# Kernel tuning notes

Measured on AMD Instinct MI355X. Metric: run time of the kernel, lower is better.

The kernel has to match this reference:

```python
import jax, jax.numpy as jnp
import numpy as np

T = 2048        # Tmax encoder frames
EPROJS = 1024   # encoder projection dim (Henc)
DUNITS = 512    # prediction net hidden
EMBED = 512     # embedding dim
JOINT = 512     # joint space dim
ODIM = 10000    # output vocab
BLANK = 0


def setup_inputs() -> dict:
    key = jax.random.key(0)
    ks = jax.random.split(key, 11)
    def g(k, shape, scale):
        return (jax.random.normal(k, shape, dtype=jnp.float32) * scale)
    inp = {
        'h': jax.random.normal(ks[0], (T, EPROJS), dtype=jnp.float32),
        # Embedding with padding_idx=blank -> blank row zeroed
        'embed': g(ks[1], (ODIM, EMBED), 0.05).at[BLANK].set(0.0),
        # LSTMCell params (torch gate order: i, f, g, o)
        'W_ih': g(ks[2], (4 * DUNITS, EMBED), 1.0 / np.sqrt(EMBED)),
        'W_hh': g(ks[3], (4 * DUNITS, DUNITS), 1.0 / np.sqrt(DUNITS)),
        'b_ih': g(ks[4], (4 * DUNITS,), 0.01),
        'b_hh': g(ks[5], (4 * DUNITS,), 0.01),
        # joint network
        'W_enc': g(ks[6], (JOINT, EPROJS), 1.0 / np.sqrt(EPROJS)),
        'b_enc': g(ks[7], (JOINT,), 0.01),
        'W_dec': g(ks[8], (JOINT, DUNITS), 1.0 / np.sqrt(DUNITS)),  # no bias
        'W_out': g(ks[9], (ODIM, JOINT), 1.0 / np.sqrt(JOINT)),
        'b_out': g(ks[10], (ODIM,), 0.01),
    }
    return inp


def _lstm_cell(x, h_prev, c_prev, W_ih, W_hh, b_ih, b_hh):
    gates = W_ih @ x + b_ih + W_hh @ h_prev + b_hh  # (4*DUNITS,)
    i, f, g, o = jnp.split(gates, 4)
    c = jax.nn.sigmoid(f) * c_prev + jax.nn.sigmoid(i) * jnp.tanh(g)
    h = jax.nn.sigmoid(o) * jnp.tanh(c)
    return h, c


def reference(h, embed, W_ih, W_hh, b_ih, b_hh, W_enc, b_enc, W_dec, W_out, b_out):
    # Precompute encoder-side joint projection (same math, hoisted out of loop)
    h_proj = h @ W_enc.T + b_enc  # (T, JOINT)

    # Initial prediction-net step on zero embedding from zero state
    zeros_e = jnp.zeros((EMBED,), dtype=h.dtype)
    zeros_d = jnp.zeros((DUNITS,), dtype=h.dtype)
    y0, c0 = _lstm_cell(zeros_e, zeros_d, zeros_d, W_ih, W_hh, b_ih, b_hh)

    def step(carry, hp_t):
        y, c, score = carry
        # joint: tanh(lin_enc(h_t) + lin_dec(y)) -> lin_out -> log_softmax
        ytu = jax.nn.log_softmax(W_out @ jnp.tanh(hp_t + W_dec @ y) + b_out)
        logp = jnp.max(ytu)
        pred = jnp.argmax(ytu)
        emitted = pred != BLANK
        # Candidate prediction-net update with embedded token
        ey = embed[pred]
        y_new, c_new = _lstm_cell(ey, y, c, W_ih, W_hh, b_ih, b_hh)
        y = jnp.where(emitted, y_new, y)
        c = jnp.where(emitted, c_new, c)
        score = score + jnp.where(emitted, logp, jnp.zeros_like(logp))
        tok = jnp.where(emitted, pred, BLANK).astype(jnp.int32)
        return (y, c, score), tok

    (y, c, score), yseq = jax.lax.scan(step, (y0, c0, jnp.float32(0.0)), h_proj)
    # yseq: (T,) int32, BLANK where no symbol was emitted at that frame
    return yseq, score
```

## Files before the change

### kernel.cpp

```cpp
#include <hip/hip_runtime.h>
#include <stdint.h>

typedef unsigned long long u64;
typedef uint32_t u32;

#define NB     256
#define NT     256
#define TMAX   2048
#define EPROJS 1024
#define DUNITS 512
#define EMBED  512
#define JOINT  512
#define ODIM   10000

#define N_LSTM 32
#define CONS0  32
#define N_CONS 223
#define AGG_B  255
#define MAGIC  0xD07ED07Eu

#define WS_Y    0
#define WS_U    4096
#define WS_PK   8192
#define WS_SA   15360
#define WS_DN   22528
#define WS_CNT  23552
#define WS_HP   32768

__device__ __forceinline__ float aloadf(const float* p){
  return __hip_atomic_load(p, __ATOMIC_RELAXED, __HIP_MEMORY_SCOPE_AGENT);
}
__device__ __forceinline__ void astoref(float* p, float v){
  __hip_atomic_store(p, v, __ATOMIC_RELAXED, __HIP_MEMORY_SCOPE_AGENT);
}
__device__ __forceinline__ u64 aloadu64(const u64* p){
  return __hip_atomic_load(p, __ATOMIC_RELAXED, __HIP_MEMORY_SCOPE_AGENT);
}
__device__ __forceinline__ void astoreu64(u64* p, u64 v){
  __hip_atomic_store(p, v, __ATOMIC_RELAXED, __HIP_MEMORY_SCOPE_AGENT);
}
__device__ __forceinline__ u32 aloadu32(const u32* p){
  return __hip_atomic_load(p, __ATOMIC_RELAXED, __HIP_MEMORY_SCOPE_AGENT);
}
__device__ __forceinline__ void astoreu32(u32* p, u32 v){
  __hip_atomic_store(p, v, __ATOMIC_RELAXED, __HIP_MEMORY_SCOPE_AGENT);
}

__device__ __forceinline__ u32 ordbits(float f){
  u32 u = __float_as_uint(f);
  return (u & 0x80000000u) ? ~u : (u | 0x80000000u);
}
__device__ __forceinline__ float unordbits(u32 o){
  u32 u = (o & 0x80000000u) ? (o & 0x7fffffffu) : ~o;
  return __uint_as_float(u);
}
__device__ __forceinline__ float sigmoidf_(float x){ return 1.0f/(1.0f+expf(-x)); }

__device__ __forceinline__ float wredsum(float v){
  #pragma unroll
  for (int o=32;o>0;o>>=1) v += __shfl_xor(v, o);
  return v;
}
__device__ __forceinline__ u64 wredmax64(u64 v){
  #pragma unroll
  for (int o=32;o>0;o>>=1){ u64 x = __shfl_xor(v, o); v = (x>v)?x:v; }
  return v;
}

#define LOAD8(dst, baseptr) { const float4* _p=(const float4*)(baseptr); \
  float4 _a=_p[0], _b=_p[1]; \
  dst[0]=_a.x; dst[1]=_a.y; dst[2]=_a.z; dst[3]=_a.w; \
  dst[4]=_b.x; dst[5]=_b.y; dst[6]=_b.z; dst[7]=_b.w; }

#define LDS8(dst, base) { float4 _a=*(const float4*)(base); \
  float4 _b=*(const float4*)((base)+4); \
  dst[0]=_a.x; dst[1]=_a.y; dst[2]=_a.z; dst[3]=_a.w; \
  dst[4]=_b.x; dst[5]=_b.y; dst[6]=_b.z; dst[7]=_b.w; }

__global__ void rnnt_init(char* ws){
  u32* p = (u32*)ws;
  for (int i = threadIdx.x; i < 8192; i += blockDim.x) p[i] = 0u;
}

__global__ void __launch_bounds__(NT, 1)
rnnt_decode(const float* __restrict__ h,    const float* __restrict__ embed,
            const float* __restrict__ W_ih, const float* __restrict__ W_hh,
            const float* __restrict__ b_ih, const float* __restrict__ b_hh,
            const float* __restrict__ W_enc,const float* __restrict__ b_enc,
            const float* __restrict__ W_dec,const float* __restrict__ W_out,
            const float* __restrict__ b_out,
            float* __restrict__ out, char* __restrict__ ws)
{
  const int b    = blockIdx.x;
  const int tid  = threadIdx.x;
  const int lane = tid & 63;
  const int w    = tid >> 6;

  float* ybuf = (float*)(ws + WS_Y);
  float* ubuf = (float*)(ws + WS_U);
  u64*  pkall = (u64*)(ws + WS_PK);
  u64*  saall = (u64*)(ws + WS_SA);
  u32*  done  = (u32*)(ws + WS_DN);
  u32*  cnt   = (u32*)(ws + WS_CNT);
  float* hp   = (float*)(ws + WS_HP);

  __shared__ float smem[8192];
  float* PL = smem;
  float* EL = &smem[4416];
  float* YL = &smem[4928];
  float* ZL = &smem[5440];
  float* GL = &smem[5952];
  u64*   R64= (u64*)&smem[6016];
  float* RF = &smem[6024];
  float* YO = &smem[6032];

  {
    float (*lds_h)[EPROJS] = (float(*)[EPROJS])smem;
    #pragma unroll
    for (int r=0;r<8;r++){
      const float4 hv = *(const float4*)(h + (size_t)(8*b + r)*EPROJS + tid*4);
      *(float4*)&lds_h[r][tid*4] = hv;
    }
    __syncthreads();
    for (int p=0;p<2;p++){
      const int j = p*NT + tid;
      float acc[8] = {0,0,0,0,0,0,0,0};
      const float4* wrow = (const float4*)(W_enc + (size_t)j*EPROJS);
      for (int k4=0;k4<EPROJS/4;k4++){
        const float4 wv = wrow[k4];
        #pragma unroll
        for (int t8=0;t8<8;t8++){
          const float4 hv = *(const float4*)&lds_h[t8][k4*4];
          acc[t8] = fmaf(wv.x,hv.x, fmaf(wv.y,hv.y, fmaf(wv.z,hv.z, fmaf(wv.w,hv.w, acc[t8]))));
        }
      }
      const float be = b_enc[j];
      #pragma unroll
      for (int t8=0;t8<8;t8++)
        astoref(&hp[(size_t)(8*b+t8)*JOINT + j], acc[t8] + be);
    }
    asm volatile("s_waitcnt vmcnt(0)" ::: "memory");
    if (tid==0) astoreu32(&done[b], MAGIC);
    __syncthreads();
  }

  if (b < N_LSTM){
    const int d = b;
    float wih[16][8], whh[16][8];
    #pragma unroll
    for (int q=0;q<16;q++){
      const int gr = w*DUNITS + 16*d + q;
      LOAD8(wih[q], W_ih + (size_t)gr*EMBED  + lane*8);
      LOAD8(whh[q], W_hh + (size_t)gr*DUNITS + lane*8);
    }
    float wdc0[16], wdc1[16];
    {
      const float4* p0 = (const float4*)(W_dec + (size_t)(2*tid)*DUNITS   + 16*d);
      const float4* p1 = (const float4*)(W_dec + (size_t)(2*tid+1)*DUNITS + 16*d);
      #pragma unroll
      for (int k4=0;k4<4;k4++){
        const float4 a = p0[k4];
        wdc0[4*k4+0]=a.x; wdc0[4*k4+1]=a.y; wdc0[4*k4+2]=a.z; wdc0[4*k4+3]=a.w;
        const float4 c = p1[k4];
        wdc1[4*k4+0]=c.x; wdc1[4*k4+1]=c.y; wdc1[4*k4+2]=c.z; wdc1[4*k4+3]=c.w;
      }
    }
    float bias_r = 0.0f;
    if (tid < 64){
      const int gr = (tid>>4)*DUNITS + 16*d + (tid&15);
      bias_r = b_ih[gr] + b_hh[gr];
    }
    float c_st = 0.0f, y_st = 0.0f;
    if (tid < 16){
      const int j = 16*d + tid;
      const float gi = b_ih[j]            + b_hh[j];
      const float gg = b_ih[2*DUNITS + j] + b_hh[2*DUNITS + j];
      const float go = b_ih[3*DUNITS + j] + b_hh[3*DUNITS + j];
      c_st = sigmoidf_(gi)*tanhf(gg);
      y_st = sigmoidf_(go)*tanhf(c_st);
      YO[tid] = y_st;
      astoref(&ybuf[512 + j], y_st);
    }
    __syncthreads();
    {
      float p0=0.f, p1=0.f;
      #pragma unroll
      for (int k=0;k<16;k++){ p0 = fmaf(wdc0[k], YO[k], p0); p1 = fmaf(wdc1[k], YO[k], p1); }
      atomicAdd(&ubuf[512 + 2*tid],   p0);
      atomicAdd(&ubuf[512 + 2*tid+1], p1);
    }
    asm volatile("s_waitcnt vmcnt(0)" ::: "memory");
    __syncthreads();
    if (tid < 8) atomicAdd(&cnt[tid*32], 1u);

    for (int t=0;t<TMAX;t++){
      const u32 g = (u32)(t+1);
      if (tid==0){ while (aloadu32(&cnt[(d&7)*32]) < 32u*g) {} }
      __syncthreads();
      {
        const u64* y64 = (const u64*)(ws + WS_Y + (g&1)*2048);
        const u64 v = aloadu64(&y64[tid]);
        YL[2*tid]   = __uint_as_float((u32)v);
        YL[2*tid+1] = __uint_as_float((u32)(v>>32));
      }
      __syncthreads();
      float y8[8]; LDS8(y8, &YL[8*lane]);
      float vp[16];
      #pragma unroll
      for (int q=0;q<16;q++){
        float a=0.f;
        #pragma unroll
        for (int k=0;k<8;k++) a = fmaf(whh[q][k], y8[k], a);
        vp[q] = a;
      }
      u64 pk = 0;
      {
        const u64* pks = pkall + (g&3)*224;
        for(;;){
          pk = (tid < N_CONS) ? aloadu64(&pks[tid]) : 0;
          const int ok = (tid < N_CONS) ? ((u32)(pk>>48) >= g) : 1;
          if (__all(ok)) break;
        }
      }
      { u64 m = wredmax64(pk); if (lane==0) R64[w]=m; }
      __syncthreads();
      u64 best = R64[0];
      #pragma unroll
      for (int i=1;i<4;i++){ const u64 x=R64[i]; best = (x>best)?x:best; }
      const int pred = (int)((~(u32)best) & 0xFFFFu);
      const int emitted = (pred != 0);
      if (tid < 16) astoref(&ubuf[(g&1)*512 + 16*d + tid], 0.0f);
      {
        const float2 ev = *(const float2*)(embed + (size_t)pred*EMBED + 2*tid);
        EL[2*tid] = ev.x; EL[2*tid+1] = ev.y;
      }
      __syncthreads();
      float e8[8]; LDS8(e8, &EL[8*lane]);
      #pragma unroll
      for (int q=0;q<16;q++){
        float a = vp[q];
        #pragma unroll
        for (int k=0;k<8;k++) a = fmaf(wih[q][k], e8[k], a);
        PL[(w*16+q)*68 + lane] = a;
      }
      __syncthreads();
      if (tid < 64){
        const float* row = &PL[tid*68];
        float s = bias_r;
        #pragma unroll
        for (int k4=0;k4<16;k4++){
          const float4 v4 = *(const float4*)&row[4*k4];
          s += v4.x + v4.y + v4.z + v4.w;
        }
        GL[tid] = s;
      }
      __syncthreads();
      if (tid < 16){
        const float gi=GL[tid], gf=GL[16+tid], gg=GL[32+tid], go=GL[48+tid];
        const float cn = sigmoidf_(gf)*c_st + sigmoidf_(gi)*tanhf(gg);
        const float yn = sigmoidf_(go)*tanhf(cn);
        if (emitted){ c_st = cn; y_st = yn; }
        YO[tid] = y_st;
        astoref(&ybuf[((g+1)&1)*512 + 16*d + tid], y_st);
      }
      __syncthreads();
      if (t < TMAX-1){
        float p0=0.f, p1=0.f;
        #pragma unroll
        for (int k=0;k<16;k++){ p0 = fmaf(wdc0[k], YO[k], p0); p1 = fmaf(wdc1[k], YO[k], p1); }
        float* up = &ubuf[((g+1)&1)*512];
        atomicAdd(&up[2*tid],   p0);
        atomicAdd(&up[2*tid+1], p1);
      }
      asm volatile("s_waitcnt vmcnt(0)" ::: "memory");
      __syncthreads();
      if (t < TMAX-1 && tid < 8) atomicAdd(&cnt[tid*32], 1u);
    }
  }
  else if (b < AGG_B){
    const int cb = b - CONS0;
    int rowstart, rowcnt;
    if (cb < 188){ rowstart = cb*45;                 rowcnt = 45; }
    else         { rowstart = 8460 + (cb-188)*44;    rowcnt = 44; }
    float wout[12][8];
    #pragma unroll
    for (int q=0;q<12;q++){
      const int s = 12*w + q;
      if (s < rowcnt){
        LOAD8(wout[q], W_out + (size_t)(rowstart+s)*JOINT + lane*8);
      } else {
        #pragma unroll
        for (int k=0;k<8;k++) wout[q][k]=0.f;
      }
    }
    float my_bo = 0.f; int my_row = 0; bool my_val = false;
    if (tid < rowcnt){ my_val = true; my_row = rowstart + tid; my_bo = b_out[my_row]; }

    for(;;){
      const u32 dv = aloadu32(&done[tid]);
      if (__all(dv == MAGIC)) break;
    }
    __syncthreads();

    const u32* cp = &cnt[(cb&7)*32];
    for (int t=0;t<TMAX;t++){
      const u32 g = (u32)(t+1);
      const float h0 = aloadf(&hp[(size_t)t*JOINT + 2*tid]);
      const float h1 = aloadf(&hp[(size_t)t*JOINT + 2*tid + 1]);
      if (tid==0){ while (aloadu32(cp) < 32u*g) {} }
      __syncthreads();
      const u64 uv = aloadu64(&((const u64*)(ws + WS_U + (g&1)*2048))[tid]);
      const float u0 = __uint_as_float((u32)uv);
      const float u1 = __uint_as_float((u32)(uv>>32));
      ZL[2*tid]   = tanhf(h0 + u0);
      ZL[2*tid+1] = tanhf(h1 + u1);
      __syncthreads();
      float z8[8]; LDS8(z8, &ZL[8*lane]);
      #pragma unroll
      for (int q=0;q<12;q++){
        float a=0.f;
        #pragma unroll
        for (int k=0;k<8;k++) a = fmaf(wout[q][k], z8[k], a);
        PL[(12*w+q)*68 + lane] = a;
      }
      __syncthreads();
      u64 key = 0; float lg = 0.f;
      if (tid < 48){
        const float* row = &PL[tid*68];
        float s = my_bo;
        #pragma unroll
        for (int k4=0;k4<16;k4++){
          const float4 v4 = *(const float4*)&row[4*k4];
          s += v4.x + v4.y + v4.z + v4.w;
        }
        lg = s;
        if (my_val) key = ((u64)ordbits(lg)<<16) | (u64)(0xFFFFu & ~(u32)my_row);
      }
      if (w == 0){
        const u64 bk = wredmax64(key);
        const float mw = unordbits((u32)(bk>>16));
        const float e  = my_val ? __expf(lg - mw) : 0.f;
        const float sw = wredsum(e);
        if (lane == 0){
          astoreu64(&saall[(g&3)*224 + cb], ((u64)g<<32) | (u64)__float_as_uint(sw));
          astoreu64(&pkall[(g&3)*224 + cb], ((u64)g<<48) | bk);
        }
      }
    }
  }
  else {
    float score = 0.0f;
    for (int t=0;t<TMAX;t++){
      const u32 g = (u32)(t+1);
      const u64* pks = pkall + (g&3)*224;
      const u64* sas = saall + (g&3)*224;
      u64 pk=0, sa=0;
      for(;;){
        if (tid < N_CONS){ pk = aloadu64(&pks[tid]); sa = aloadu64(&sas[tid]); }
        const int ok = (tid < N_CONS) ? (((u32)(pk>>48) >= g) & ((u32)(sa>>32) >= g)) : 1;
        if (__all(ok)) break;
      }
      { u64 m = wredmax64(pk); if (lane==0) R64[w]=m; }
      __syncthreads();
      u64 best = R64[0];
      #pragma unroll
      for (int i=1;i<4;i++){ const u64 x=R64[i]; best = (x>best)?x:best; }
      const float mstar = unordbits((u32)(best>>16));
      float term = (tid < N_CONS) ?
        __uint_as_float((u32)sa) * __expf(unordbits((u32)(pk>>16)) - mstar) : 0.f;
      term = wredsum(term);
      if (lane==0) RF[w] = term;
      __syncthreads();
      if (tid==0){
        const float S = RF[0]+RF[1]+RF[2]+RF[3];
        const int pred = (int)((~(u32)best) & 0xFFFFu);
        if (pred != 0) score += -logf(S);
        out[t] = (float)pred;
      }
      __syncthreads();
    }
    if (tid==0) out[TMAX] = score;
  }
}

extern "C" void kernel_launch(void* const* d_in, const int* in_sizes, int n_in,
                              void* d_out, int out_size, void* d_ws, size_t ws_size,
                              hipStream_t stream)
{
  const float* h     = (const float*)d_in[0];
  const float* embed = (const float*)d_in[1];
  const float* W_ih  = (const float*)d_in[2];
  const float* W_hh  = (const float*)d_in[3];
  const float* b_ih  = (const float*)d_in[4];
  const float* b_hh  = (const float*)d_in[5];
  const float* W_enc = (const float*)d_in[6];
  const float* b_enc = (const float*)d_in[7];
  const float* W_dec = (const float*)d_in[8];
  const float* W_out = (const float*)d_in[9];
  const float* b_out = (const float*)d_in[10];
  float* out = (float*)d_out;
  char* ws = (char*)d_ws;

  hipLaunchKernelGGL(rnnt_init, dim3(1), dim3(NT), 0, stream, ws);
  hipLaunchKernelGGL(rnnt_decode, dim3(NB), dim3(NT), 0, stream,
                     h, embed, W_ih, W_hh, b_ih, b_hh, W_enc, b_enc, W_dec, W_out, b_out,
                     out, ws);
}
```

Measured before the change: 16.98 ms.

## Compute decoder projection from gathered y with a separate counter to shorten critical path

Each LSTM block now reads the full previous y vector directly into registers, computes its 16 rows of W_dec·y with wave reductions, stores them with plain stores instead of atomicAdd accumulation, and signals the output blocks through a new second counter. The output blocks wait on that counter rather than the LSTM-finished counter, so the joint computation can start before the LSTM cell update finishes. Several LDS staging round-trips and barriers are replaced by direct per-lane global loads, and the embedding row is prefetched speculatively from the per-wave argmax before the block-wide reduction. In exchange every LSTM block reads all of y each step, and the output blocks add a trailing barrier.

After: 21.39 ms. 25.9% more time.

```diff
diff --git a/kernel.cpp b/kernel.cpp
--- a/kernel.cpp
+++ b/kernel.cpp
@@ -25,6 +25,7 @@
 #define WS_SA   15360
 #define WS_DN   22528
 #define WS_CNT  23552
+#define WS_CNT2 24576
 #define WS_HP   32768
 
 __device__ __forceinline__ float aloadf(const float* p){
@@ -69,11 +70,6 @@
 
 #define LOAD8(dst, baseptr) { const float4* _p=(const float4*)(baseptr); \
   float4 _a=_p[0], _b=_p[1]; \
-  dst[0]=_a.x; dst[1]=_a.y; dst[2]=_a.z; dst[3]=_a.w; \
-  dst[4]=_b.x; dst[5]=_b.y; dst[6]=_b.z; dst[7]=_b.w; }
-
-#define LDS8(dst, base) { float4 _a=*(const float4*)(base); \
-  float4 _b=*(const float4*)((base)+4); \
   dst[0]=_a.x; dst[1]=_a.y; dst[2]=_a.z; dst[3]=_a.w; \
   dst[4]=_b.x; dst[5]=_b.y; dst[6]=_b.z; dst[7]=_b.w; }
 
@@ -97,22 +93,18 @@
   const int w    = tid >> 6;
 
   float* ybuf = (float*)(ws + WS_Y);
-  float* ubuf = (float*)(ws + WS_U);
   u64*  pkall = (u64*)(ws + WS_PK);
   u64*  saall = (u64*)(ws + WS_SA);
   u32*  done  = (u32*)(ws + WS_DN);
   u32*  cnt   = (u32*)(ws + WS_CNT);
+  u32*  cnt2  = (u32*)(ws + WS_CNT2);
   float* hp   = (float*)(ws + WS_HP);
 
   __shared__ float smem[8192];
   float* PL = smem;
-  float* EL = &smem[4416];
-  float* YL = &smem[4928];
-  float* ZL = &smem[5440];
-  float* GL = &smem[5952];
-  u64*   R64= (u64*)&smem[6016];
-  float* RF = &smem[6024];
-  float* YO = &smem[6032];
+  float* GL = &smem[4416];
+  u64*   R64= (u64*)&smem[4480];
+  float* RF = &smem[4488];
 
   {
     float (*lds_h)[EPROJS] = (float(*)[EPROJS])smem;
@@ -153,17 +145,11 @@
       LOAD8(wih[q], W_ih + (size_t)gr*EMBED  + lane*8);
       LOAD8(whh[q], W_hh + (size_t)gr*DUNITS + lane*8);
     }
-    float wdc0[16], wdc1[16];
-    {
-      const float4* p0 = (const float4*)(W_dec + (size_t)(2*tid)*DUNITS   + 16*d);
-      const float4* p1 = (const float4*)(W_dec + (size_t)(2*tid+1)*DUNITS + 16*d);
-      #pragma unroll
-      for (int k4=0;k4<4;k4++){
-        const float4 a = p0[k4];
-        wdc0[4*k4+0]=a.x; wdc0[4*k4+1]=a.y; wdc0[4*k4+2]=a.z; wdc0[4*k4+3]=a.w;
-        const float4 c = p1[k4];
-        wdc1[4*k4+0]=c.x; wdc1[4*k4+1]=c.y; wdc1[4*k4+2]=c.z; wdc1[4*k4+3]=c.w;
-      }
+    float wdr[4][8];
+    #pragma unroll
+    for (int i=0;i<4;i++){
+      const int r = 16*d + 4*w + i;
+      LOAD8(wdr[i], W_dec + (size_t)r*DUNITS + 8*lane);
     }
     float bias_r = 0.0f;
     if (tid < 64){
@@ -178,33 +164,48 @@
       const float go = b_ih[3*DUNITS + j] + b_hh[3*DUNITS + j];
       c_st = sigmoidf_(gi)*tanhf(gg);
       y_st = sigmoidf_(go)*tanhf(c_st);
-      YO[tid] = y_st;
       astoref(&ybuf[512 + j], y_st);
     }
-    __syncthreads();
-    {
-      float p0=0.f, p1=0.f;
-      #pragma unroll
-      for (int k=0;k<16;k++){ p0 = fmaf(wdc0[k], YO[k], p0); p1 = fmaf(wdc1[k], YO[k], p1); }
-      atomicAdd(&ubuf[512 + 2*tid],   p0);
-      atomicAdd(&ubuf[512 + 2*tid+1], p1);
-    }
     asm volatile("s_waitcnt vmcnt(0)" ::: "memory");
-    __syncthreads();
     if (tid < 8) atomicAdd(&cnt[tid*32], 1u);
 
     for (int t=0;t<TMAX;t++){
       const u32 g = (u32)(t+1);
       if (tid==0){ while (aloadu32(&cnt[(d&7)*32]) < 32u*g) {} }
       __syncthreads();
+      float y8[8];
       {
-        const u64* y64 = (const u64*)(ws + WS_Y + (g&1)*2048);
-        const u64 v = aloadu64(&y64[tid]);
-        YL[2*tid]   = __uint_as_float((u32)v);
-        YL[2*tid+1] = __uint_as_float((u32)(v>>32));
-      }
-      __syncthreads();
-      float y8[8]; LDS8(y8, &YL[8*lane]);
+        const u64* yb = (const u64*)(ws + WS_Y + (size_t)(g&1)*2048);
+        #pragma unroll
+        for (int i=0;i<4;i++){
+          const u64 v = aloadu64(&yb[4*lane + i]);
+          y8[2*i]   = __uint_as_float((u32)v);
+          y8[2*i+1] = __uint_as_float((u32)(v>>32));
+        }
+      }
+      {
+        float p0=0.f,p1=0.f,p2=0.f,p3=0.f;
+        #pragma unroll
+        for (int k=0;k<8;k++){
+          p0 = fmaf(wdr[0][k], y8[k], p0);
+          p1 = fmaf(wdr[1][k], y8[k], p1);
+          p2 = fmaf(wdr[2][k], y8[k], p2);
+          p3 = fmaf(wdr[3][k], y8[k], p3);
+        }
+        #pragma unroll
+        for (int o=32;o>0;o>>=1){
+          p0 += __shfl_xor(p0,o); p1 += __shfl_xor(p1,o);
+          p2 += __shfl_xor(p2,o); p3 += __shfl_xor(p3,o);
+        }
+        if (lane==0){
+          float* up = (float*)(ws + WS_U + (size_t)(g&1)*2048) + 16*d + 4*w;
+          astoref(&up[0],p0); astoref(&up[1],p1);
+          astoref(&up[2],p2); astoref(&up[3],p3);
+        }
+      }
+      asm volatile("s_waitcnt vmcnt(0)" ::: "memory");
+      __syncthreads();
+      if (tid < 8) atomicAdd(&cnt2[tid*32], 1u);
       float vp[16];
       #pragma unroll
       for (int q=0;q<16;q++){
@@ -222,20 +223,20 @@
           if (__all(ok)) break;
         }
       }
-      { u64 m = wredmax64(pk); if (lane==0) R64[w]=m; }
+      const u64 m = wredmax64(pk);
+      if (lane==0) R64[w] = m;
+      const int predw = (int)((~(u32)m) & 0xFFFFu);
+      float e8[8];
+      LOAD8(e8, embed + (size_t)predw*EMBED + 8*lane);
       __syncthreads();
       u64 best = R64[0];
       #pragma unroll
       for (int i=1;i<4;i++){ const u64 x=R64[i]; best = (x>best)?x:best; }
       const int pred = (int)((~(u32)best) & 0xFFFFu);
       const int emitted = (pred != 0);
-      if (tid < 16) astoref(&ubuf[(g&1)*512 + 16*d + tid], 0.0f);
-      {
-        const float2 ev = *(const float2*)(embed + (size_t)pred*EMBED + 2*tid);
-        EL[2*tid] = ev.x; EL[2*tid+1] = ev.y;
-      }
-      __syncthreads();
-      float e8[8]; LDS8(e8, &EL[8*lane]);
+      if (m != best){
+        LOAD8(e8, embed + (size_t)pred*EMBED + 8*lane);
+      }
       #pragma unroll
       for (int q=0;q<16;q++){
         float a = vp[q];
@@ -260,20 +261,9 @@
         const float cn = sigmoidf_(gf)*c_st + sigmoidf_(gi)*tanhf(gg);
         const float yn = sigmoidf_(go)*tanhf(cn);
         if (emitted){ c_st = cn; y_st = yn; }
-        YO[tid] = y_st;
         astoref(&ybuf[((g+1)&1)*512 + 16*d + tid], y_st);
       }
-      __syncthreads();
-      if (t < TMAX-1){
-        float p0=0.f, p1=0.f;
-        #pragma unroll
-        for (int k=0;k<16;k++){ p0 = fmaf(wdc0[k], YO[k], p0); p1 = fmaf(wdc1[k], YO[k], p1); }
-        float* up = &ubuf[((g+1)&1)*512];
-        atomicAdd(&up[2*tid],   p0);
-        atomicAdd(&up[2*tid+1], p1);
-      }
       asm volatile("s_waitcnt vmcnt(0)" ::: "memory");
-      __syncthreads();
       if (t < TMAX-1 && tid < 8) atomicAdd(&cnt[tid*32], 1u);
     }
   }
@@ -302,20 +292,23 @@
     }
     __syncthreads();
 
-    const u32* cp = &cnt[(cb&7)*32];
+    const u32* cp2 = &cnt2[(cb&7)*32];
     for (int t=0;t<TMAX;t++){
       const u32 g = (u32)(t+1);
-      const float h0 = aloadf(&hp[(size_t)t*JOINT + 2*tid]);
-      const float h1 = aloadf(&hp[(size_t)t*JOINT + 2*tid + 1]);
-      if (tid==0){ while (aloadu32(cp) < 32u*g) {} }
-      __syncthreads();
-      const u64 uv = aloadu64(&((const u64*)(ws + WS_U + (g&1)*2048))[tid]);
-      const float u0 = __uint_as_float((u32)uv);
-      const float u1 = __uint_as_float((u32)(uv>>32));
-      ZL[2*tid]   = tanhf(h0 + u0);
-      ZL[2*tid+1] = tanhf(h1 + u1);
-      __syncthreads();
-      float z8[8]; LDS8(z8, &ZL[8*lane]);
+      float h8[8];
+      LOAD8(h8, hp + (size_t)t*JOINT + 8*lane);
+      if (tid==0){ while (aloadu32(cp2) < 32u*g) {} }
+      __syncthreads();
+      float z8[8];
+      {
+        const u64* ub = (const u64*)(ws + WS_U + (size_t)(g&1)*2048);
+        #pragma unroll
+        for (int i=0;i<4;i++){
+          const u64 v = aloadu64(&ub[4*lane + i]);
+          z8[2*i]   = tanhf(h8[2*i]   + __uint_as_float((u32)v));
+          z8[2*i+1] = tanhf(h8[2*i+1] + __uint_as_float((u32)(v>>32)));
+        }
+      }
       #pragma unroll
       for (int q=0;q<12;q++){
         float a=0.f;
@@ -346,6 +339,7 @@
           astoreu64(&pkall[(g&3)*224 + cb], ((u64)g<<48) | bk);
         }
       }
+      __syncthreads();
     }
   }
   else {
```
